# Performance work log

Measured on AMD Instinct MI355X. Metric: run time of the kernel, lower is better.

## Reference

```python
import jax, jax.numpy as jnp
import numpy as np

B, L, D_MODEL, N_HEADS = 8, 256, 2048, 8
D_HEAD = D_MODEL // N_HEADS  # 256 == L, required by DeltaRuleOperator broadcasting
ALPHA0, BETA0 = 0.1, 0.9      # delta_rule_strength, 1 - strength
LN_EPS = 1e-5


def setup_inputs() -> dict:
    k = jax.random.key(0)
    ks = jax.random.split(k, 8)
    s = 0.02
    return {
        "query": jax.random.normal(ks[0], (B, L, D_MODEL), jnp.float32),
        "key": jax.random.normal(ks[1], (B, L, D_MODEL), jnp.float32),
        "value": jax.random.normal(ks[2], (B, L, D_MODEL), jnp.float32),
        "Wq": jax.random.normal(ks[3], (D_MODEL, D_MODEL), jnp.float32) * s,
        "Wk": jax.random.normal(ks[4], (D_MODEL, D_MODEL), jnp.float32) * s,
        "Wv": jax.random.normal(ks[5], (D_MODEL, D_MODEL), jnp.float32) * s,
        "Wo": jax.random.normal(ks[6], (D_MODEL, D_MODEL), jnp.float32) * s,
        "bo": jnp.zeros((D_MODEL,), jnp.float32),
        "ln_g": jnp.ones((D_MODEL,), jnp.float32),
        "ln_b": jnp.zeros((D_MODEL,), jnp.float32),
        "alpha": jnp.asarray(ALPHA0, jnp.float32),
        "beta": jnp.asarray(BETA0, jnp.float32),
    }


def reference(query, key, value, Wq, Wk, Wv, Wo, bo, ln_g, ln_b, alpha, beta):
    Bs, Ls, D = query.shape
    H, Dh = N_HEADS, D // N_HEADS

    def proj(x, W):  # torch Linear: x @ W.T, split heads -> [B,H,L,Dh]
        return (x @ W.T).reshape(Bs, Ls, H, Dh).transpose(0, 2, 1, 3)

    Q = proj(query, Wq)
    K = proj(key, Wk)
    V = proj(value, Wv)

    # DeltaRuleOperator, applied sequentially per head (buffer mutates across heads)
    kv = jnp.einsum('bhld,bhmd->bhlm', K, V)  # [B,H,L,L] with L == Dh
    kv_heads = jnp.moveaxis(kv, 1, 0)          # [H,B,L,L]

    def cs_step(cs, kv_h):
        # cumulative_state = beta*cs + alpha*detach(mean(kv)); head uses pre-update cs
        new = beta * cs + alpha * jax.lax.stop_gradient(kv_h.mean(axis=(0, 1)))
        return new, cs

    _, cs_seq = jax.lax.scan(cs_step, jnp.zeros((Dh,), query.dtype), kv_heads)  # [H,Dh]
    cs_b = cs_seq[None, :, None, :]                       # [1,H,1,Dh]
    q_mod = Q * (cs_b + alpha * (kv - cs_b))              # delta-rule modulated queries

    # elu feature map
    phi = lambda x: jax.nn.elu(x) + 1.0
    pq, pk = phi(q_mod), phi(K)

    def time_major(x):  # [B,H,L,Dh] -> [L, B*H, Dh]
        return x.reshape(Bs * H, Ls, Dh).transpose(1, 0, 2)

    pq_t, pk_t, v_t = time_major(pq), time_major(pk), time_major(V)

    def step(carry, xs):
        S, Z = carry                        # S:[N,Dh,Dh], Z:[N,Dh]
        q_i, k_i, v_i = xs                  # each [N,Dh]
        S = S + k_i[:, :, None] * v_i[:, None, :]
        Z = Z + k_i
        num = jnp.einsum('nf,nfd->nd', q_i, S)
        den = jnp.maximum(jnp.sum(q_i * Z, axis=-1), 1e-8)
        return (S, Z), num / den[:, None]

    N = Bs * H
    S0 = jnp.zeros((N, Dh, Dh), query.dtype)
    Z0 = jnp.zeros((N, Dh), query.dtype)
    _, outs = jax.lax.scan(step, (S0, Z0), (pq_t, pk_t, v_t))  # [L,N,Dh]

    attn = outs.transpose(1, 0, 2).reshape(Bs, H, Ls, Dh)
    attn = attn.transpose(0, 2, 1, 3).reshape(Bs, Ls, D)       # concat heads

    o = attn @ Wo.T + bo                  # out_proj (dropout is identity in eval)
    x = query + o                          # residual + LayerNorm
    mu = x.mean(-1, keepdims=True)
    var = jnp.mean((x - mu) ** 2, axis=-1, keepdims=True)
    return (x - mu) / jnp.sqrt(var + LN_EPS) * ln_g + ln_b
```

## Files before the change

### kernel.cpp

```cpp
#include <hip/hip_runtime.h>
#include <hip/hip_bf16.h>

using u16 = unsigned short;

typedef __bf16 bf16x8 __attribute__((ext_vector_type(8)));
typedef float  f32x4  __attribute__((ext_vector_type(4)));

__device__ __forceinline__ float b2f(u16 u) {
  union { unsigned u; float f; } v; v.u = ((unsigned)u) << 16; return v.f;
}
__device__ __forceinline__ u16 f2b(float f) {
  union { float f; unsigned u; } v; v.f = f;
  unsigned r = v.u + 0x7fffu + ((v.u >> 16) & 1u);
  return (u16)(r >> 16);
}

__device__ __forceinline__ void gld_lds16(const void* g, void* l) {
  __builtin_amdgcn_global_load_lds(
      (__attribute__((address_space(1))) void*)(unsigned long long)(g),
      (__attribute__((address_space(3))) void*)(unsigned long long)(l),
      16, 0, 0);
}

template <int EPI, int BK>
__global__ __launch_bounds__(256) void gemm_bt(
    const u16* __restrict__ A, int lda, long sA1, long sA2,
    const u16* __restrict__ B, int ldb, long sB1, long sB2,
    void* __restrict__ Cv, int ldc, long sC1, long sC2,
    int K, int HDIV,
    const float* __restrict__ bias, const float* __restrict__ resid,
    float* __restrict__ partOut) {
  __shared__ __align__(16) u16 lds[2 * 128 * BK];
  __shared__ float denS[128];
  const int t = threadIdx.x;
  const int lane = t & 63;
  const int wave = t >> 6;
  const int wm = wave >> 1, wn = wave & 1;
  const int laneM = lane & 15, quad = lane >> 4;
  const int zb = blockIdx.z / HDIV, zh = blockIdx.z % HDIV;

  int bx = blockIdx.x, by = blockIdx.y;
  if (EPI == 2) { by = (bx >= 1) ? 1 : 0; bx = (bx == 2) ? 1 : 0; }
  const int kEnd = (EPI == 3) ? ((by + 1) * 128 < K ? (by + 1) * 128 : K) : K;

  const u16* Abase = A + zb * sA1 + zh * sA2 + (long)by * 128 * lda;
  const u16* Bbase = B + zb * sB1 + zh * sB2 + (long)bx * 128 * ldb;

  constexpr int STEPS = BK / 16;
  constexpr int RPS = 2048 / BK;
  constexpr int KK = BK / 32;
  const int sRow = (BK == 64) ? (t >> 3) : (t >> 2);
  const int sg = (BK == 64) ? (t & 7) : (t & 3);
  const int swz = (BK == 64) ? (sg ^ (sRow & 7)) : (sg ^ ((sRow >> 1) & 3));
  const int sc = swz * 8;

  f32x4 acc[4][4];
#pragma unroll
  for (int i = 0; i < 4; ++i)
#pragma unroll
    for (int j = 0; j < 4; ++j) acc[i][j] = (f32x4){0.f, 0.f, 0.f, 0.f};
  float dsum[4] = {0.f, 0.f, 0.f, 0.f};

  for (int k0 = 0; k0 < kEnd; k0 += BK) {
#pragma unroll
    for (int p = 0; p < STEPS; ++p)
      gld_lds16(Abase + (long)(p * RPS + sRow) * lda + k0 + sc,
                &lds[p * 2048 + t * 8]);
#pragma unroll
    for (int p = 0; p < STEPS; ++p)
      gld_lds16(Bbase + (long)(p * RPS + sRow) * ldb + k0 + sc,
                &lds[128 * BK + p * 2048 + t * 8]);
    __syncthreads();
    bf16x8 af[KK][4], bfv[KK][4];
#pragma unroll
    for (int kk = 0; kk < KK; ++kk) {
      int perm8;
      if (BK == 64) perm8 = ((kk * 4 + quad) ^ (laneM & 7)) * 8;
      else          perm8 = (quad ^ ((laneM >> 1) & 3)) * 8;
#pragma unroll
      for (int i = 0; i < 4; ++i) {
        af[kk][i] = *(const bf16x8*)&lds[(wm * 64 + i * 16 + laneM) * BK + perm8];
        bfv[kk][i] =
            *(const bf16x8*)&lds[128 * BK + (wn * 64 + i * 16 + laneM) * BK + perm8];
      }
    }
    if (EPI == 3) {
#pragma unroll
      for (int kk = 0; kk < KK; ++kk)
#pragma unroll
        for (int i = 0; i < 4; ++i) {
          union { bf16x8 v; u16 s[8]; } u; u.v = af[kk][i];
          float ds = 0.f;
#pragma unroll
          for (int e = 0; e < 8; ++e) ds += b2f(u.s[e]);
          dsum[i] += ds;
        }
    }
#pragma unroll
    for (int kk = 0; kk < KK; ++kk)
#pragma unroll
      for (int i = 0; i < 4; ++i)
#pragma unroll
        for (int j = 0; j < 4; ++j)
          acc[i][j] = __builtin_amdgcn_mfma_f32_16x16x32_bf16(
              af[kk][i], bfv[kk][j], acc[i][j], 0, 0, 0);
    __syncthreads();
  }

  if (EPI == 3) {
#pragma unroll
    for (int i = 0; i < 4; ++i) {
      float s = dsum[i];
      s += __shfl_xor(s, 16);
      s += __shfl_xor(s, 32);
      if (wn == 0 && quad == 0)
        denS[wm * 64 + i * 16 + laneM] = fmaxf(s, 1e-8f);
    }
    __syncthreads();
  }

  if (EPI == 1) {
#pragma unroll
    for (int j = 0; j < 4; ++j) {
      float s = 0.f;
#pragma unroll
      for (int i = 0; i < 4; ++i)
#pragma unroll
        for (int r = 0; r < 4; ++r) s += acc[i][j][r];
      s += __shfl_xor(s, 16);
      s += __shfl_xor(s, 32);
      if (quad == 0)
        atomicAdd(&partOut[zh * 256 + bx * 128 + wn * 64 + j * 16 + laneM], s);
    }
  }

  const long cOff = zb * sC1 + zh * sC2;
  const int colB = bx * 128 + wn * 64;
#pragma unroll
  for (int i = 0; i < 4; ++i) {
#pragma unroll
    for (int j = 0; j < 4; ++j) {
#pragma unroll
      for (int r = 0; r < 4; ++r) {
        const int lrow = wm * 64 + i * 16 + quad * 4 + r;
        const int row = by * 128 + lrow;
        const int col = colB + j * 16 + laneM;
        const long idx = cOff + (long)row * ldc + col;
        float v = acc[i][j][r];
        if (EPI == 0 || EPI == 1) {
          ((u16*)Cv)[idx] = f2b(v);
        } else if (EPI == 2) {
          ((u16*)Cv)[idx] = f2b(col <= row ? v : 0.0f);
        } else if (EPI == 3) {
          ((u16*)Cv)[idx] = f2b(v / denS[lrow]);
        } else {
          ((float*)Cv)[idx] =
              (zb == 0) ? v + bias[col] + resid[(long)row * ldc + col] : v;
        }
      }
    }
  }
}

template <int EPI>
__global__ __launch_bounds__(512) void gemm256(
    const u16* __restrict__ A, int lda, long sA1,
    const u16* __restrict__ B, int ldb, long sB1,
    void* __restrict__ Cv, int ldc, long sC1, int K,
    const float* __restrict__ bias, const float* __restrict__ resid) {
  __shared__ __align__(16) u16 ldsA[3][8192];
  __shared__ __align__(16) u16 ldsB[3][8192];
  const int t = threadIdx.x;
  const int lane = t & 63, wave = t >> 6;
  const int wm = wave >> 2, wn = wave & 3;
  const int laneM = lane & 15, quad = lane >> 4;

  const int cpx = gridDim.x >> 3;
  const int id2 = (blockIdx.x & 7) * cpx + (blockIdx.x >> 3);
  const int bx = id2 & 7, by = (id2 >> 3) & 7, z = id2 >> 6;

  const u16* Ag = A + (long)z * sA1 + (long)by * 256 * lda;
  const u16* Bg = B + (long)z * sB1 + (long)bx * 256 * ldb;

  const int nt = K >> 5;
  const int rg = (quad ^ ((laneM >> 1) & 3)) * 8;
  const int rowA = wm * 128 + laneM;
  const int rowB = wn * 64 + laneM;

  f32x4 acc[8][4];
#pragma unroll
  for (int i = 0; i < 8; ++i)
#pragma unroll
    for (int j = 0; j < 4; ++j) acc[i][j] = (f32x4){0.f, 0.f, 0.f, 0.f};

  {
#pragma unroll
    for (int p = 0; p < 2; ++p) {
      const int chunk = p * 512 + t, row = chunk >> 2;
      const int c = (chunk & 3) ^ ((row >> 1) & 3);
      gld_lds16(Ag + row * lda + c * 8, &ldsA[0][chunk * 8]);
    }
#pragma unroll
    for (int p = 0; p < 2; ++p) {
      const int chunk = p * 512 + t, row = chunk >> 2;
      const int c = (chunk & 3) ^ ((row >> 1) & 3);
      gld_lds16(Bg + row * ldb + c * 8, &ldsB[0][chunk * 8]);
    }
#pragma unroll
    for (int p = 0; p < 2; ++p) {
      const int chunk = p * 512 + t, row = chunk >> 2;
      const int c = (chunk & 3) ^ ((row >> 1) & 3);
      gld_lds16(Ag + row * lda + 32 + c * 8, &ldsA[1][chunk * 8]);
    }
#pragma unroll
    for (int p = 0; p < 2; ++p) {
      const int chunk = p * 512 + t, row = chunk >> 2;
      const int c = (chunk & 3) ^ ((row >> 1) & 3);
      gld_lds16(Bg + row * ldb + 32 + c * 8, &ldsB[1][chunk * 8]);
    }
  }
  asm volatile("s_waitcnt vmcnt(4)" ::: "memory");
  __builtin_amdgcn_s_barrier();

  int buf = 0, sbuf = 2;
  for (int tau = 0; tau < nt; ++tau) {
    const u16* la = &ldsA[buf][0];
    const u16* lb = &ldsB[buf][0];
    const bool st = (tau + 2) < nt;
    const int ks = (tau + 2) << 5;
    bf16x8 af[4], bv[4];

#pragma unroll
    for (int m = 0; m < 4; ++m)
      af[m] = *(const bf16x8*)&la[(rowA + m * 16) * 32 + rg];
#pragma unroll
    for (int n = 0; n < 4; ++n)
      bv[n] = *(const bf16x8*)&lb[(rowB + n * 16) * 32 + rg];
    if (st) {
#pragma unroll
      for (int p = 0; p < 2; ++p) {
        const int chunk = p * 512 + t, row = chunk >> 2;
        const int c = (chunk & 3) ^ ((row >> 1) & 3);
        gld_lds16(Ag + row * lda + ks + c * 8, &ldsA[sbuf][chunk * 8]);
      }
    }
    __builtin_amdgcn_s_barrier();
    asm volatile("s_waitcnt lgkmcnt(0)" ::: "memory");
    __builtin_amdgcn_s_setprio(1);
#pragma unroll
    for (int m = 0; m < 4; ++m)
#pragma unroll
      for (int n = 0; n < 4; ++n)
        acc[m][n] = __builtin_amdgcn_mfma_f32_16x16x32_bf16(af[m], bv[n],
                                                            acc[m][n], 0, 0, 0);
    __builtin_amdgcn_s_setprio(0);
    __builtin_amdgcn_s_barrier();

#pragma unroll
    for (int m = 0; m < 4; ++m)
      af[m] = *(const bf16x8*)&la[(rowA + 64 + m * 16) * 32 + rg];
    if (st) {
#pragma unroll
      for (int p = 0; p < 2; ++p) {
        const int chunk = p * 512 + t, row = chunk >> 2;
        const int c = (chunk & 3) ^ ((row >> 1) & 3);
        gld_lds16(Bg + row * ldb + ks + c * 8, &ldsB[sbuf][chunk * 8]);
      }
    }
    __builtin_amdgcn_s_barrier();
    asm volatile("s_waitcnt lgkmcnt(0)" ::: "memory");
    __builtin_amdgcn_s_setprio(1);
#pragma unroll
    for (int m = 0; m < 4; ++m)
#pragma unroll
      for (int n = 0; n < 4; ++n)
        acc[4 + m][n] = __builtin_amdgcn_mfma_f32_16x16x32_bf16(
            af[m], bv[n], acc[4 + m][n], 0, 0, 0);
    __builtin_amdgcn_s_setprio(0);

    if (tau < nt - 1) {
      if (st) asm volatile("s_waitcnt vmcnt(4)" ::: "memory");
      else    asm volatile("s_waitcnt vmcnt(0)" ::: "memory");
      __builtin_amdgcn_s_barrier();
    }
    buf = (buf == 2) ? 0 : buf + 1;
    sbuf = (sbuf == 2) ? 0 : sbuf + 1;
  }

  const long cOff = (long)z * sC1;
  const int colB = bx * 256 + wn * 64;
  const int rowBase = by * 256 + wm * 128;
#pragma unroll
  for (int i = 0; i < 8; ++i) {
#pragma unroll
    for (int j = 0; j < 4; ++j) {
#pragma unroll
      for (int r = 0; r < 4; ++r) {
        const int row = rowBase + i * 16 + quad * 4 + r;
        const int col = colB + j * 16 + laneM;
        const long idx = cOff + (long)row * ldc + col;
        float v = acc[i][j][r];
        if (EPI == 0) {
          ((u16*)Cv)[idx] = f2b(v);
        } else {
          ((float*)Cv)[idx] =
              (z == 0) ? v + bias[col] + resid[(long)row * ldc + col] : v;
        }
      }
    }
  }
}

__global__ __launch_bounds__(256) void convert7(
    const float* __restrict__ s0, const float* __restrict__ s1,
    const float* __restrict__ s2, const float* __restrict__ s3,
    const float* __restrict__ s4, const float* __restrict__ s5,
    const float* __restrict__ s6, u16* __restrict__ dst) {
  long idx = (long)blockIdx.x * 256 + threadIdx.x;
  int seg = (int)(idx >> 20);
  long off = (idx & 1048575) << 2;
  const float* s;
  switch (seg) {
    case 0: s = s0; break; case 1: s = s1; break; case 2: s = s2; break;
    case 3: s = s3; break; case 4: s = s4; break; case 5: s = s5; break;
    default: s = s6;
  }
  float4 v = *(const float4*)(s + off);
  ushort4 o;
  o.x = f2b(v.x); o.y = f2b(v.y); o.z = f2b(v.z); o.w = f2b(v.w);
  *(ushort4*)(dst + (long)seg * 4194304 + off) = o;
}

__global__ __launch_bounds__(256) void cs_kernel(
    const float* __restrict__ part, float* __restrict__ cs,
    const float* __restrict__ alphaP, const float* __restrict__ betaP) {
  int m = threadIdx.x;
  float alpha = *alphaP, beta = *betaP;
  float c = 0.f;
  for (int h = 0; h < 8; ++h) {
    cs[h * 256 + m] = c;
    c = beta * c + alpha * (part[h * 256 + m] * (1.0f / 2048.0f));
  }
}

__global__ __launch_bounds__(256) void pqpk_kernel(
    const u16* __restrict__ Qp, const u16* __restrict__ Kp,
    const u16* __restrict__ kv, const float* __restrict__ cs,
    const float* __restrict__ alphaP, u16* __restrict__ pq,
    u16* __restrict__ pk) {
  long idx = (long)blockIdx.x * 256 + threadIdx.x;
  int d = idx & 255, l = (int)((idx >> 8) & 255), h = (int)((idx >> 16) & 7),
      b = (int)(idx >> 19);
  float alpha = *alphaP;
  long pidx = ((long)(b * 256 + l)) * 2048 + h * 256 + d;
  float Qv = b2f(Qp[pidx]);
  float kvv = b2f(kv[idx]);
  float csv = cs[h * 256 + d];
  float qm = Qv * (csv + alpha * (kvv - csv));
  pq[idx] = f2b(qm > 0.f ? qm + 1.f : expf(qm));
  float Kv = b2f(Kp[pidx]);
  pk[idx] = f2b(Kv > 0.f ? Kv + 1.f : expf(Kv));
}

__global__ __launch_bounds__(256) void vtrans_kernel(const u16* __restrict__ Vp,
                                                     u16* __restrict__ Vt) {
  __shared__ u16 tile[32][33];
  int z = blockIdx.z, b = z >> 3, h = z & 7;
  int jT = blockIdx.x * 32, dT = blockIdx.y * 32;
  int tx = threadIdx.x, ty = threadIdx.y;
#pragma unroll
  for (int ii = 0; ii < 4; ++ii) {
    int j = jT + ty + ii * 8, d = dT + tx;
    tile[ty + ii * 8][tx] = Vp[(long)(b * 256 + j) * 2048 + h * 256 + d];
  }
  __syncthreads();
#pragma unroll
  for (int ii = 0; ii < 4; ++ii) {
    int d = dT + ty + ii * 8, j = jT + tx;
    Vt[(long)z * 65536 + d * 256 + j] = tile[tx][ty + ii * 8];
  }
}

__global__ __launch_bounds__(256) void ln_kernel(
    const float* __restrict__ x0, const float* __restrict__ x1,
    const float* __restrict__ g, const float* __restrict__ bb,
    float* __restrict__ out) {
  int row = blockIdx.x, t = threadIdx.x;
  const float4* xr0 = (const float4*)(x0 + (long)row * 2048);
  const float4* xr1 = (const float4*)(x1 + (long)row * 2048);
  float4 a0 = xr0[t], b0 = xr1[t], a1 = xr0[t + 256], b1 = xr1[t + 256];
  float4 v0, v1;
  v0.x = a0.x + b0.x; v0.y = a0.y + b0.y; v0.z = a0.z + b0.z; v0.w = a0.w + b0.w;
  v1.x = a1.x + b1.x; v1.y = a1.y + b1.y; v1.z = a1.z + b1.z; v1.w = a1.w + b1.w;
  float s = v0.x + v0.y + v0.z + v0.w + v1.x + v1.y + v1.z + v1.w;
  float ss = v0.x * v0.x + v0.y * v0.y + v0.z * v0.z + v0.w * v0.w +
             v1.x * v1.x + v1.y * v1.y + v1.z * v1.z + v1.w * v1.w;
  for (int o = 32; o; o >>= 1) { s += __shfl_xor(s, o); ss += __shfl_xor(ss, o); }
  __shared__ float a1s[4], a2s[4];
  int wave = t >> 6, lane = t & 63;
  if (lane == 0) { a1s[wave] = s; a2s[wave] = ss; }
  __syncthreads();
  s = a1s[0] + a1s[1] + a1s[2] + a1s[3];
  ss = a2s[0] + a2s[1] + a2s[2] + a2s[3];
  float mu = s * (1.f / 2048.f);
  float var = ss * (1.f / 2048.f) - mu * mu;
  float rstd = rsqrtf(var + 1e-5f);
  const float4* g4 = (const float4*)g;
  const float4* b4 = (const float4*)bb;
  float4* orow = (float4*)(out + (long)row * 2048);
  float4 gg = g4[t], bv = b4[t], r;
  r.x = (v0.x - mu) * rstd * gg.x + bv.x;
  r.y = (v0.y - mu) * rstd * gg.y + bv.y;
  r.z = (v0.z - mu) * rstd * gg.z + bv.z;
  r.w = (v0.w - mu) * rstd * gg.w + bv.w;
  orow[t] = r;
  gg = g4[t + 256]; bv = b4[t + 256];
  r.x = (v1.x - mu) * rstd * gg.x + bv.x;
  r.y = (v1.y - mu) * rstd * gg.y + bv.y;
  r.z = (v1.z - mu) * rstd * gg.z + bv.z;
  r.w = (v1.w - mu) * rstd * gg.w + bv.w;
  orow[t + 256] = r;
}

extern "C" void kernel_launch(void* const* d_in, const int* in_sizes, int n_in,
                              void* d_out, int out_size, void* d_ws,
                              size_t ws_size, hipStream_t stream) {
  const float* query = (const float*)d_in[0];
  const float* key = (const float*)d_in[1];
  const float* value = (const float*)d_in[2];
  const float* Wq = (const float*)d_in[3];
  const float* Wk = (const float*)d_in[4];
  const float* Wv = (const float*)d_in[5];
  const float* Wo = (const float*)d_in[6];
  const float* bo = (const float*)d_in[7];
  const float* ln_g = (const float*)d_in[8];
  const float* ln_b = (const float*)d_in[9];
  const float* alphaP = (const float*)d_in[10];
  const float* betaP = (const float*)d_in[11];

  char* ws = (char*)d_ws;
  const long SZ = 8388608;
  u16* qb = (u16*)(ws);
  u16* Wb = (u16*)(ws + 3 * SZ);
  u16* Qp = (u16*)(ws + 7 * SZ);
  u16* kvb = (u16*)(ws + 10 * SZ);
  u16* pq = (u16*)(ws + 12 * SZ);
  u16* pk = (u16*)(ws + 13 * SZ);
  u16* Vt = (u16*)(ws + 14 * SZ);
  u16* attnb = (u16*)(ws + 15 * SZ);
  u16* Ab = (u16*)(ws + 10 * SZ);
  float* x0 = (float*)(ws + 12 * SZ);
  float* x1 = (float*)(ws);
  float* part = (float*)(ws + 16 * SZ);
  float* cs = (float*)(ws + 16 * SZ + 16384);

  u16* Kp = Qp + 4194304;
  u16* Vp = Qp + 8388608;
  u16* Wob = Wb + 3 * 4194304;

  hipMemsetAsync(part, 0, 8 * 256 * sizeof(float), stream);

  convert7<<<28672, 256, 0, stream>>>(query, key, value, Wq, Wk, Wv, Wo, qb);

  gemm256<0><<<dim3(192, 1, 1), 512, 0, stream>>>(
      qb, 2048, 4194304L, Wb, 2048, 4194304L, (void*)Qp, 2048, 4194304L,
      2048, nullptr, nullptr);

  gemm_bt<1, 64><<<dim3(2, 2, 64), 256, 0, stream>>>(
      Kp, 2048, 524288L, 256L, Vp, 2048, 524288L, 256L, (void*)kvb, 256,
      524288L, 65536L, 256, 8, nullptr, nullptr, part);

  cs_kernel<<<1, 256, 0, stream>>>(part, cs, alphaP, betaP);

  pqpk_kernel<<<16384, 256, 0, stream>>>(Qp, Kp, kvb, cs, alphaP, pq, pk);

  gemm_bt<2, 64><<<dim3(3, 1, 64), 256, 0, stream>>>(
      pq, 256, 524288L, 65536L, pk, 256, 524288L, 65536L, (void*)Ab, 256,
      524288L, 65536L, 256, 8, nullptr, nullptr, nullptr);

  vtrans_kernel<<<dim3(8, 8, 64), dim3(32, 8), 0, stream>>>(Vp, Vt);

  gemm_bt<3, 64><<<dim3(2, 2, 64), 256, 0, stream>>>(
      Ab, 256, 524288L, 65536L, Vt, 256, 524288L, 65536L, (void*)attnb, 2048,
      524288L, 256L, 256, 8, nullptr, nullptr, nullptr);

  gemm256<4><<<dim3(128, 1, 1), 512, 0, stream>>>(
      attnb, 2048, 1024L, Wob, 2048, 1024L, (void*)x0, 2048, -25165824L,
      1024, bo, query);

  ln_kernel<<<2048, 256, 0, stream>>>(x0, x1, ln_g, ln_b, (float*)d_out);
}
```

Baseline: 344.2 us.

## Deepen gemm256 LDS pipeline to four stages with static buffers

Changes the 256x256 GEMM from a 3-stage to a 4-stage LDS ring, prefetching three k-tiles ahead instead of two. The loop is unrolled by four with separately named static LDS buffers, which removes the runtime buffer index arithmetic, and global source addresses are precomputed once per thread. The goal is to hide more global-load latency and cut address math in the inner loop. In exchange, LDS use grows to 128KB per block, and the unrolled loop requires nt to be a multiple of 4 or it reads past the staged tiles.

```diff
diff --git a/kernel.cpp b/kernel.cpp
--- a/kernel.cpp
+++ b/kernel.cpp
@@ -162,14 +162,71 @@
   }
 }
 
+__device__ __forceinline__ void g256_tile(
+    const u16* __restrict__ la, const u16* __restrict__ lb,
+    u16* __restrict__ sa, u16* __restrict__ sb, int tau, int nt,
+    const u16* AgR0, const u16* AgR1, const u16* BgR0, const u16* BgR1,
+    int rowA, int rowB, int rg, int t, f32x4 (&acc)[8][4]) {
+  const bool st = (tau + 3) < nt;
+  const int ks = (tau + 3) << 5;
+  bf16x8 af[4], bv[4];
+#pragma unroll
+  for (int m = 0; m < 4; ++m)
+    af[m] = *(const bf16x8*)&la[(rowA + m * 16) * 32 + rg];
+#pragma unroll
+  for (int n = 0; n < 4; ++n)
+    bv[n] = *(const bf16x8*)&lb[(rowB + n * 16) * 32 + rg];
+  if (st) {
+    gld_lds16(AgR0 + ks, &sa[t * 8]);
+    gld_lds16(AgR1 + ks, &sa[4096 + t * 8]);
+  }
+  __builtin_amdgcn_s_barrier();
+  asm volatile("s_waitcnt lgkmcnt(0)" ::: "memory");
+  __builtin_amdgcn_s_setprio(1);
+#pragma unroll
+  for (int m = 0; m < 4; ++m)
+#pragma unroll
+    for (int n = 0; n < 4; ++n)
+      acc[m][n] = __builtin_amdgcn_mfma_f32_16x16x32_bf16(af[m], bv[n],
+                                                          acc[m][n], 0, 0, 0);
+  __builtin_amdgcn_s_setprio(0);
+  __builtin_amdgcn_s_barrier();
+#pragma unroll
+  for (int m = 0; m < 4; ++m)
+    af[m] = *(const bf16x8*)&la[(rowA + 64 + m * 16) * 32 + rg];
+  if (st) {
+    gld_lds16(BgR0 + ks, &sb[t * 8]);
+    gld_lds16(BgR1 + ks, &sb[4096 + t * 8]);
+  }
+  __builtin_amdgcn_s_barrier();
+  asm volatile("s_waitcnt lgkmcnt(0)" ::: "memory");
+  __builtin_amdgcn_s_setprio(1);
+#pragma unroll
+  for (int m = 0; m < 4; ++m)
+#pragma unroll
+    for (int n = 0; n < 4; ++n)
+      acc[4 + m][n] = __builtin_amdgcn_mfma_f32_16x16x32_bf16(
+          af[m], bv[n], acc[4 + m][n], 0, 0, 0);
+  __builtin_amdgcn_s_setprio(0);
+  if (tau < nt - 1) {
+    if (tau + 3 < nt)
+      asm volatile("s_waitcnt vmcnt(8)" ::: "memory");
+    else if (tau + 2 < nt)
+      asm volatile("s_waitcnt vmcnt(4)" ::: "memory");
+    else
+      asm volatile("s_waitcnt vmcnt(0)" ::: "memory");
+    __builtin_amdgcn_s_barrier();
+  }
+}
+
 template <int EPI>
 __global__ __launch_bounds__(512) void gemm256(
     const u16* __restrict__ A, int lda, long sA1,
     const u16* __restrict__ B, int ldb, long sB1,
     void* __restrict__ Cv, int ldc, long sC1, int K,
     const float* __restrict__ bias, const float* __restrict__ resid) {
-  __shared__ __align__(16) u16 ldsA[3][8192];
-  __shared__ __align__(16) u16 ldsB[3][8192];
+  __shared__ __align__(16) u16 A0[8192], A1[8192], A2[8192], A3[8192];
+  __shared__ __align__(16) u16 B0[8192], B1[8192], B2[8192], B3[8192];
   const int t = threadIdx.x;
   const int lane = t & 63, wave = t >> 6;
   const int wm = wave >> 2, wn = wave & 3;
@@ -187,104 +244,38 @@
   const int rowA = wm * 128 + laneM;
   const int rowB = wn * 64 + laneM;
 
+  const int sRow0 = t >> 2, sRow1 = (512 + t) >> 2;
+  const int sc0 = (((t) & 3) ^ ((sRow0 >> 1) & 3)) * 8;
+  const int sc1 = (((512 + t) & 3) ^ ((sRow1 >> 1) & 3)) * 8;
+  const u16* AgR0 = Ag + (long)sRow0 * lda + sc0;
+  const u16* AgR1 = Ag + (long)sRow1 * lda + sc1;
+  const u16* BgR0 = Bg + (long)sRow0 * ldb + sc0;
+  const u16* BgR1 = Bg + (long)sRow1 * ldb + sc1;
+
   f32x4 acc[8][4];
 #pragma unroll
   for (int i = 0; i < 8; ++i)
 #pragma unroll
     for (int j = 0; j < 4; ++j) acc[i][j] = (f32x4){0.f, 0.f, 0.f, 0.f};
 
-  {
-#pragma unroll
-    for (int p = 0; p < 2; ++p) {
-      const int chunk = p * 512 + t, row = chunk >> 2;
-      const int c = (chunk & 3) ^ ((row >> 1) & 3);
-      gld_lds16(Ag + row * lda + c * 8, &ldsA[0][chunk * 8]);
-    }
-#pragma unroll
-    for (int p = 0; p < 2; ++p) {
-      const int chunk = p * 512 + t, row = chunk >> 2;
-      const int c = (chunk & 3) ^ ((row >> 1) & 3);
-      gld_lds16(Bg + row * ldb + c * 8, &ldsB[0][chunk * 8]);
-    }
-#pragma unroll
-    for (int p = 0; p < 2; ++p) {
-      const int chunk = p * 512 + t, row = chunk >> 2;
-      const int c = (chunk & 3) ^ ((row >> 1) & 3);
-      gld_lds16(Ag + row * lda + 32 + c * 8, &ldsA[1][chunk * 8]);
-    }
-#pragma unroll
-    for (int p = 0; p < 2; ++p) {
-      const int chunk = p * 512 + t, row = chunk >> 2;
-      const int c = (chunk & 3) ^ ((row >> 1) & 3);
-      gld_lds16(Bg + row * ldb + 32 + c * 8, &ldsB[1][chunk * 8]);
-    }
-  }
-  asm volatile("s_waitcnt vmcnt(4)" ::: "memory");
+  gld_lds16(AgR0, &A0[t * 8]);      gld_lds16(AgR1, &A0[4096 + t * 8]);
+  gld_lds16(BgR0, &B0[t * 8]);      gld_lds16(BgR1, &B0[4096 + t * 8]);
+  gld_lds16(AgR0 + 32, &A1[t * 8]); gld_lds16(AgR1 + 32, &A1[4096 + t * 8]);
+  gld_lds16(BgR0 + 32, &B1[t * 8]); gld_lds16(BgR1 + 32, &B1[4096 + t * 8]);
+  gld_lds16(AgR0 + 64, &A2[t * 8]); gld_lds16(AgR1 + 64, &A2[4096 + t * 8]);
+  gld_lds16(BgR0 + 64, &B2[t * 8]); gld_lds16(BgR1 + 64, &B2[4096 + t * 8]);
+  asm volatile("s_waitcnt vmcnt(8)" ::: "memory");
   __builtin_amdgcn_s_barrier();
 
-  int buf = 0, sbuf = 2;
-  for (int tau = 0; tau < nt; ++tau) {
-    const u16* la = &ldsA[buf][0];
-    const u16* lb = &ldsB[buf][0];
-    const bool st = (tau + 2) < nt;
-    const int ks = (tau + 2) << 5;
-    bf16x8 af[4], bv[4];
-
-#pragma unroll
-    for (int m = 0; m < 4; ++m)
-      af[m] = *(const bf16x8*)&la[(rowA + m * 16) * 32 + rg];
-#pragma unroll
-    for (int n = 0; n < 4; ++n)
-      bv[n] = *(const bf16x8*)&lb[(rowB + n * 16) * 32 + rg];
-    if (st) {
-#pragma unroll
-      for (int p = 0; p < 2; ++p) {
-        const int chunk = p * 512 + t, row = chunk >> 2;
-        const int c = (chunk & 3) ^ ((row >> 1) & 3);
-        gld_lds16(Ag + row * lda + ks + c * 8, &ldsA[sbuf][chunk * 8]);
-      }
-    }
-    __builtin_amdgcn_s_barrier();
-    asm volatile("s_waitcnt lgkmcnt(0)" ::: "memory");
-    __builtin_amdgcn_s_setprio(1);
-#pragma unroll
-    for (int m = 0; m < 4; ++m)
-#pragma unroll
-      for (int n = 0; n < 4; ++n)
-        acc[m][n] = __builtin_amdgcn_mfma_f32_16x16x32_bf16(af[m], bv[n],
-                                                            acc[m][n], 0, 0, 0);
-    __builtin_amdgcn_s_setprio(0);
-    __builtin_amdgcn_s_barrier();
-
-#pragma unroll
-    for (int m = 0; m < 4; ++m)
-      af[m] = *(const bf16x8*)&la[(rowA + 64 + m * 16) * 32 + rg];
-    if (st) {
-#pragma unroll
-      for (int p = 0; p < 2; ++p) {
-        const int chunk = p * 512 + t, row = chunk >> 2;
-        const int c = (chunk & 3) ^ ((row >> 1) & 3);
-        gld_lds16(Bg + row * ldb + ks + c * 8, &ldsB[sbuf][chunk * 8]);
-      }
-    }
-    __builtin_amdgcn_s_barrier();
-    asm volatile("s_waitcnt lgkmcnt(0)" ::: "memory");
-    __builtin_amdgcn_s_setprio(1);
-#pragma unroll
-    for (int m = 0; m < 4; ++m)
-#pragma unroll
-      for (int n = 0; n < 4; ++n)
-        acc[4 + m][n] = __builtin_amdgcn_mfma_f32_16x16x32_bf16(
-            af[m], bv[n], acc[4 + m][n], 0, 0, 0);
-    __builtin_amdgcn_s_setprio(0);
-
-    if (tau < nt - 1) {
-      if (st) asm volatile("s_waitcnt vmcnt(4)" ::: "memory");
-      else    asm volatile("s_waitcnt vmcnt(0)" ::: "memory");
-      __builtin_amdgcn_s_barrier();
-    }
-    buf = (buf == 2) ? 0 : buf + 1;
-    sbuf = (sbuf == 2) ? 0 : sbuf + 1;
+  for (int tau = 0; tau < nt; tau += 4) {
+    g256_tile(A0, B0, A3, B3, tau, nt, AgR0, AgR1, BgR0, BgR1, rowA, rowB,
+              rg, t, acc);
+    g256_tile(A1, B1, A0, B0, tau + 1, nt, AgR0, AgR1, BgR0, BgR1, rowA,
+              rowB, rg, t, acc);
+    g256_tile(A2, B2, A1, B1, tau + 2, nt, AgR0, AgR1, BgR0, BgR1, rowA,
+              rowB, rg, t, acc);
+    g256_tile(A3, B3, A2, B2, tau + 3, nt, AgR0, AgR1, BgR0, BgR1, rowA,
+              rowB, rg, t, acc);
   }
 
   const long cOff = (long)z * sC1;
```

After: 335.0 us. 1.03x faster.
